# Kernel optimization log

Measured on AMD Instinct MI355X. Metric: run time of the kernel, lower is better.

Reference implementation:

```python
import jax, jax.numpy as jnp
import numpy as np

GROUP = 64      # quantization group size along the K (in_features) dim
QMAX = 7.0      # symmetric signed int4 range [-7, 7]


def fake_quant_w4a4(t):
    """Per-group symmetric int4 fake-quantization along last dim (STE-friendly).

    t: [..., K] with K % GROUP == 0. Emulates nunchaku's quantize_w4a4
    numerics: scale = max|group| / 7, q = clip(round(t/scale)) * scale.
    """
    shp = t.shape
    g = t.reshape(shp[:-1] + (shp[-1] // GROUP, GROUP))
    scale = jnp.maximum(jnp.max(jnp.abs(g), axis=-1, keepdims=True) / QMAX, 1e-8)
    q = jnp.clip(jnp.round(g / scale), -QMAX, QMAX) * scale
    # straight-through estimator so gradients flow through the quant branch
    q = g + jax.lax.stop_gradient(q - g)
    return q.reshape(shp)


def setup_inputs() -> dict:
    key = jax.random.key(0)
    k0, k1, k2, k3, k4, k5 = jax.random.split(key, 6)
    B, K, N, R = 8192, 2048, 2048, 32  # tokens, in_features, out_features, rank
    x = jax.random.normal(k0, (B, K), jnp.float32)
    residual_weight = jax.random.normal(k1, (N, K), jnp.float32) * 0.02
    lora_down = jax.random.normal(k2, (K, R), jnp.float32) * 0.02
    lora_up = jax.random.normal(k3, (N, R), jnp.float32) * 0.02
    smooth = jax.random.uniform(k4, (K,), jnp.float32, minval=0.5, maxval=2.0)
    bias = jax.random.normal(k5, (N,), jnp.float32) * 0.01
    return {"x": x, "residual_weight": residual_weight, "lora_down": lora_down,
            "lora_up": lora_up, "smooth": smooth, "bias": bias}


def reference(x, residual_weight, lora_down, lora_up, smooth, bias):
    """SVDQuant forward: W4A4 GEMM on the residual weight fused with an
    FP low-rank (SVD) correction and per-channel smoothing.

    y = Q4(x*smooth) @ Q4(W_res).T + (x*smooth) @ lora_down @ lora_up.T + bias
    """
    x_s = x * smooth                                   # [B, K] smoothed activations
    y_lr = (x_s @ lora_down) @ lora_up.T               # [B, R] -> [B, N] low-rank branch
    y_q = fake_quant_w4a4(x_s) @ fake_quant_w4a4(residual_weight).T  # int4xint4 branch
    return y_q + y_lr + bias
```

## Files before the change

kernel.cpp:

```cpp
#include <hip/hip_runtime.h>
#include <stdint.h>


typedef __attribute__((ext_vector_type(8))) short short8;
typedef __attribute__((ext_vector_type(8))) unsigned short ushort8;
typedef __attribute__((ext_vector_type(4))) unsigned short ushort4v;
typedef __attribute__((ext_vector_type(4))) float floatx4;

#define M_TOK 8192
#define K_IN  2048
#define N_OUT 2048
#define RANK  32
#define KC    2112
#define NTILE 33
#define XS_STRIDE 2056
#define XROWS 8

__device__ __forceinline__ unsigned short f2bf(float f) {
  unsigned int u = __float_as_uint(f);
  u += 0x7fff + ((u >> 16) & 1);
  return (unsigned short)(u >> 16);
}

__device__ __forceinline__ void quant8(const float* v, unsigned short* q) {
  float amax = 0.f;
#pragma unroll
  for (int i = 0; i < 8; ++i) amax = fmaxf(amax, fabsf(v[i]));
  amax = fmaxf(amax, __shfl_xor(amax, 1, 64));
  amax = fmaxf(amax, __shfl_xor(amax, 2, 64));
  amax = fmaxf(amax, __shfl_xor(amax, 4, 64));
  float scale = fmaxf(amax / 7.0f, 1e-8f);
#pragma unroll
  for (int i = 0; i < 8; ++i) {
    float qq = rintf(v[i] / scale);
    qq = fminf(fmaxf(qq, -7.f), 7.f);
    q[i] = f2bf(qq * scale);
  }
}

__global__ __launch_bounds__(256) void prep_kernel(const float* __restrict__ x,
                                                   const float* __restrict__ smooth,
                                                   const float* __restrict__ wgt,
                                                   const float* __restrict__ ld,
                                                   const float* __restrict__ lup,
                                                   unsigned short* __restrict__ Xcat,
                                                   unsigned short* __restrict__ Wcat) {
  __shared__ unsigned short xs[XROWS * XS_STRIDE];
  __shared__ float red[4][XROWS][32];
  int tid = threadIdx.x;

  if (blockIdx.x >= 1024) {
    int row = blockIdx.x - 1024;
    const float4* wr = (const float4*)(wgt + (size_t)row * K_IN);
    float4 a0 = wr[tid * 2], a1 = wr[tid * 2 + 1];
    float v[8] = {a0.x, a0.y, a0.z, a0.w, a1.x, a1.y, a1.z, a1.w};
    ushort8 q;
    quant8(v, (unsigned short*)&q);
    *(ushort8*)(Wcat + (size_t)row * KC + tid * 8) = q;
    if (tid < 32)      Wcat[(size_t)row * KC + 2048 + tid] = f2bf(lup[row * RANK + tid]);
    else if (tid < 64) Wcat[(size_t)row * KC + 2048 + tid] = 0;
    return;
  }

  int rowbase = blockIdx.x * XROWS;
  int w = tid >> 6, lane = tid & 63, quad = lane >> 4, l16 = lane & 15;

  const float4* sr = (const float4*)smooth;
  float4 s0 = sr[tid * 2], s1 = sr[tid * 2 + 1];
#pragma unroll 2
  for (int r = 0; r < XROWS; ++r) {
    const float4* xr = (const float4*)(x + (size_t)(rowbase + r) * K_IN);
    float4 a0 = xr[tid * 2], a1 = xr[tid * 2 + 1];
    float v[8] = {a0.x * s0.x, a0.y * s0.y, a0.z * s0.z, a0.w * s0.w,
                  a1.x * s1.x, a1.y * s1.y, a1.z * s1.z, a1.w * s1.w};
    ushort8 q;
    quant8(v, (unsigned short*)&q);
    *(ushort8*)(Xcat + (size_t)(rowbase + r) * KC + tid * 8) = q;
    ushort8 sb;
#pragma unroll
    for (int t = 0; t < 8; ++t) sb[t] = f2bf(v[t]);
    *(ushort8*)(xs + r * XS_STRIDE + tid * 8) = sb;
  }
  if (tid < 128)
    *(unsigned int*)(Xcat + (size_t)(rowbase + (tid >> 4)) * KC + 2080 + (tid & 15) * 2) = 0u;
  __syncthreads();

  floatx4 acc[2];
  acc[0] = (floatx4)0.f;
  acc[1] = (floatx4)0.f;
  int kbase = w * 512;
  int arow = (l16 & 7) * XS_STRIDE;
#pragma unroll 2
  for (int it = 0; it < 16; ++it) {
    int k = kbase + it * 32 + quad * 8;
    short8 af = *(const short8*)(xs + arow + k);
    short8 b0, b1;
#pragma unroll
    for (int j = 0; j < 8; ++j) {
      b0[j] = (short)f2bf(ld[(size_t)(k + j) * RANK + l16]);
      b1[j] = (short)f2bf(ld[(size_t)(k + j) * RANK + 16 + l16]);
    }
    acc[0] = __builtin_amdgcn_mfma_f32_16x16x32_bf16(af, b0, acc[0], 0, 0, 0);
    acc[1] = __builtin_amdgcn_mfma_f32_16x16x32_bf16(af, b1, acc[1], 0, 0, 0);
  }
#pragma unroll
  for (int nt = 0; nt < 2; ++nt)
#pragma unroll
    for (int r = 0; r < 4; ++r) {
      int row = quad * 4 + r;
      if (row < XROWS) red[w][row][nt * 16 + l16] = acc[nt][r];
    }
  __syncthreads();
  if (tid < 64) {
    int rl = tid >> 3, seg = tid & 7;
    ushort4v o;
#pragma unroll
    for (int j = 0; j < 4; ++j) {
      int c = seg * 4 + j;
      float s = red[0][rl][c] + red[1][rl][c] + red[2][rl][c] + red[3][rl][c];
      o[j] = f2bf(s);
    }
    *(ushort4v*)(Xcat + (size_t)(rowbase + rl) * KC + 2048 + seg * 4) = o;
  }
}

__device__ __forceinline__ void gld_lds16(const unsigned short* g, unsigned short* l) {
  __builtin_amdgcn_global_load_lds(
      (const __attribute__((address_space(1))) unsigned int*)g,
      (__attribute__((address_space(3))) unsigned int*)l, 16, 0, 0);
}

__global__ __launch_bounds__(512) void gemm_kernel(const unsigned short* __restrict__ Xcat,
                                                   const unsigned short* __restrict__ Wcat,
                                                   const float* __restrict__ bias,
                                                   float* __restrict__ out) {
  __shared__ unsigned short smem[65536];
  int tid = threadIdx.x;
  int w = tid >> 6, lane = tid & 63, quad = lane >> 4, l16 = lane & 15;
  int wm = w >> 2, wn = w & 3;

  int bid = blockIdx.x;
  int wg = (bid & 7) * 32 + (bid >> 3);
  int bM = (wg >> 3) * 256;
  int bN = (wg & 7) * 256;

  int srow = tid >> 3;
  int csrc = (tid & 7) ^ (srow & 7);
  const unsigned short* Ag = Xcat + (size_t)(bM + srow) * KC + csrc * 8;
  const unsigned short* Bg = Wcat + (size_t)(bN + srow) * KC + csrc * 8;
  int ldsrow = w * 512;

#define STAGE(tt, OFF)                                                        \
  do {                                                                        \
    int k0_ = (tt) * 64;                                                      \
    gld_lds16(Ag + k0_,            smem + (OFF) + ldsrow);                    \
    gld_lds16(Ag + 64 * KC + k0_,  smem + (OFF) + 4096 + ldsrow);             \
    gld_lds16(Ag + 128 * KC + k0_, smem + (OFF) + 8192 + ldsrow);             \
    gld_lds16(Ag + 192 * KC + k0_, smem + (OFF) + 12288 + ldsrow);            \
    gld_lds16(Bg + k0_,            smem + (OFF) + 16384 + ldsrow);            \
    gld_lds16(Bg + 64 * KC + k0_,  smem + (OFF) + 20480 + ldsrow);            \
    gld_lds16(Bg + 128 * KC + k0_, smem + (OFF) + 24576 + ldsrow);            \
    gld_lds16(Bg + 192 * KC + k0_, smem + (OFF) + 28672 + ldsrow);            \
  } while (0)

  int l7 = l16 & 7;
  int ck0 = (quad ^ l7) * 8;
  int ck1 = ((4 + quad) ^ l7) * 8;
  int aoff[8], boff[4];
#pragma unroll
  for (int mt = 0; mt < 8; ++mt) aoff[mt] = (wm * 128 + mt * 16 + l16) * 64;
#pragma unroll
  for (int nt = 0; nt < 4; ++nt) boff[nt] = 16384 + (wn * 64 + nt * 16 + l16) * 64;

  floatx4 acc[8][4];
#pragma unroll
  for (int mt = 0; mt < 8; ++mt)
#pragma unroll
    for (int nt = 0; nt < 4; ++nt) acc[mt][nt] = (floatx4)0.f;

  STAGE(0, 0);
  asm volatile("s_waitcnt vmcnt(0)" ::: "memory");
  __builtin_amdgcn_s_barrier();

#pragma unroll 1
  for (int t = 0; t < NTILE; ++t) {
    unsigned short* sb = smem + (t & 1) * 32768;

    if (t + 1 < NTILE) STAGE(t + 1, ((t + 1) & 1) * 32768);

    short8 b0[4], b1[4], a00[4], a01[4], a10[4], a11[4];

#pragma unroll
    for (int nt = 0; nt < 4; ++nt) b0[nt] = *(const short8*)(sb + boff[nt] + ck0);
#pragma unroll
    for (int mt = 0; mt < 4; ++mt) a00[mt] = *(const short8*)(sb + aoff[mt] + ck0);
#pragma unroll
    for (int mt = 0; mt < 4; ++mt) a01[mt] = *(const short8*)(sb + aoff[mt + 4] + ck0);

    __builtin_amdgcn_s_setprio(1);
#pragma unroll
    for (int mt = 0; mt < 4; ++mt)
#pragma unroll
      for (int nt = 0; nt < 4; ++nt)
        acc[mt][nt] = __builtin_amdgcn_mfma_f32_16x16x32_bf16(a00[mt], b0[nt], acc[mt][nt], 0, 0, 0);
    __builtin_amdgcn_s_setprio(0);

#pragma unroll
    for (int nt = 0; nt < 4; ++nt) b1[nt] = *(const short8*)(sb + boff[nt] + ck1);
#pragma unroll
    for (int mt = 0; mt < 4; ++mt) a10[mt] = *(const short8*)(sb + aoff[mt] + ck1);

    __builtin_amdgcn_s_setprio(1);
#pragma unroll
    for (int mt = 0; mt < 4; ++mt)
#pragma unroll
      for (int nt = 0; nt < 4; ++nt)
        acc[mt + 4][nt] = __builtin_amdgcn_mfma_f32_16x16x32_bf16(a01[mt], b0[nt], acc[mt + 4][nt], 0, 0, 0);
    __builtin_amdgcn_s_setprio(0);

#pragma unroll
    for (int mt = 0; mt < 4; ++mt) a11[mt] = *(const short8*)(sb + aoff[mt + 4] + ck1);

    __builtin_amdgcn_s_setprio(1);
#pragma unroll
    for (int mt = 0; mt < 4; ++mt)
#pragma unroll
      for (int nt = 0; nt < 4; ++nt)
        acc[mt][nt] = __builtin_amdgcn_mfma_f32_16x16x32_bf16(a10[mt], b1[nt], acc[mt][nt], 0, 0, 0);
    __builtin_amdgcn_s_setprio(0);

    __builtin_amdgcn_s_setprio(1);
#pragma unroll
    for (int mt = 0; mt < 4; ++mt)
#pragma unroll
      for (int nt = 0; nt < 4; ++nt)
        acc[mt + 4][nt] = __builtin_amdgcn_mfma_f32_16x16x32_bf16(a11[mt], b1[nt], acc[mt + 4][nt], 0, 0, 0);
    __builtin_amdgcn_s_setprio(0);

    if (t + 1 < NTILE) {
      asm volatile("s_waitcnt vmcnt(0)" ::: "memory");
      __builtin_amdgcn_s_barrier();
      __builtin_amdgcn_sched_barrier(0);
    }
  }
#undef STAGE

#pragma unroll
  for (int nt = 0; nt < 4; ++nt) {
    int col = bN + wn * 64 + nt * 16 + l16;
    float bv = bias[col];
#pragma unroll
    for (int mt = 0; mt < 8; ++mt) {
      int row = bM + wm * 128 + mt * 16 + quad * 4;
#pragma unroll
      for (int r2 = 0; r2 < 4; ++r2)
        out[(size_t)(row + r2) * N_OUT + col] = acc[mt][nt][r2] + bv;
    }
  }
}

extern "C" void kernel_launch(void* const* d_in, const int* in_sizes, int n_in,
                              void* d_out, int out_size, void* d_ws, size_t ws_size,
                              hipStream_t stream) {
  const float* x      = (const float*)d_in[0];
  const float* wgt    = (const float*)d_in[1];
  const float* ld     = (const float*)d_in[2];
  const float* lup    = (const float*)d_in[3];
  const float* smooth = (const float*)d_in[4];
  const float* bias   = (const float*)d_in[5];
  float* out = (float*)d_out;

  unsigned short* Xcat = (unsigned short*)d_ws;
  unsigned short* Wcat = Xcat + (size_t)M_TOK * KC;

  hipLaunchKernelGGL(prep_kernel, dim3(1024 + N_OUT), dim3(256), 0, stream,
                     x, smooth, wgt, ld, lup, Xcat, Wcat);
  hipLaunchKernelGGL(gemm_kernel, dim3((M_TOK / 256) * (N_OUT / 256)), dim3(512), 0, stream,
                     Xcat, Wcat, bias, out);
}
```

Baseline: 203.5 us.

## Shrink GEMM tile to 256x128, K-step 32, triple-buffer LDS for occupancy

```diff
diff --git a/kernel.cpp b/kernel.cpp
--- a/kernel.cpp
+++ b/kernel.cpp
@@ -12,7 +12,7 @@
 #define N_OUT 2048
 #define RANK  32
 #define KC    2112
-#define NTILE 33
+#define NTILE 66
 #define XS_STRIDE 2056
 #define XROWS 8
 
@@ -130,118 +130,83 @@
       (__attribute__((address_space(3))) unsigned int*)l, 16, 0, 0);
 }
 
-__global__ __launch_bounds__(512) void gemm_kernel(const unsigned short* __restrict__ Xcat,
-                                                   const unsigned short* __restrict__ Wcat,
-                                                   const float* __restrict__ bias,
-                                                   float* __restrict__ out) {
-  __shared__ unsigned short smem[65536];
+__global__ __launch_bounds__(512, 4) void gemm_kernel(const unsigned short* __restrict__ Xcat,
+                                                      const unsigned short* __restrict__ Wcat,
+                                                      const float* __restrict__ bias,
+                                                      float* __restrict__ out) {
+  __shared__ unsigned short smem[36864];
   int tid = threadIdx.x;
   int w = tid >> 6, lane = tid & 63, quad = lane >> 4, l16 = lane & 15;
-  int wm = w >> 2, wn = w & 3;
+  int wm = w >> 1, wn = w & 1;
 
   int bid = blockIdx.x;
-  int wg = (bid & 7) * 32 + (bid >> 3);
-  int bM = (wg >> 3) * 256;
-  int bN = (wg & 7) * 256;
-
-  int srow = tid >> 3;
-  int csrc = (tid & 7) ^ (srow & 7);
+  int wg = (bid & 7) * 64 + (bid >> 3);
+  int bM = (wg >> 4) * 256;
+  int bN = (wg & 15) * 128;
+
+  int srow = tid >> 2;
+  int csrc = (tid & 3) ^ ((tid >> 3) & 3);
   const unsigned short* Ag = Xcat + (size_t)(bM + srow) * KC + csrc * 8;
   const unsigned short* Bg = Wcat + (size_t)(bN + srow) * KC + csrc * 8;
-  int ldsrow = w * 512;
+  int ldsw = w * 512;
+
+  int ck = (quad ^ ((l16 >> 1) & 3)) * 8;
+  int aoff[4], boff[4];
+#pragma unroll
+  for (int mt = 0; mt < 4; ++mt) aoff[mt] = (wm * 64 + mt * 16 + l16) * 32 + ck;
+#pragma unroll
+  for (int nt = 0; nt < 4; ++nt) boff[nt] = 8192 + (wn * 64 + nt * 16 + l16) * 32 + ck;
+
+  floatx4 acc[4][4];
+#pragma unroll
+  for (int mt = 0; mt < 4; ++mt)
+#pragma unroll
+    for (int nt = 0; nt < 4; ++nt) acc[mt][nt] = (floatx4)0.f;
+
+  int b0 = 0, b1 = 12288, b2 = 24576;
 
 #define STAGE(tt, OFF)                                                        \
   do {                                                                        \
-    int k0_ = (tt) * 64;                                                      \
-    gld_lds16(Ag + k0_,            smem + (OFF) + ldsrow);                    \
-    gld_lds16(Ag + 64 * KC + k0_,  smem + (OFF) + 4096 + ldsrow);             \
-    gld_lds16(Ag + 128 * KC + k0_, smem + (OFF) + 8192 + ldsrow);             \
-    gld_lds16(Ag + 192 * KC + k0_, smem + (OFF) + 12288 + ldsrow);            \
-    gld_lds16(Bg + k0_,            smem + (OFF) + 16384 + ldsrow);            \
-    gld_lds16(Bg + 64 * KC + k0_,  smem + (OFF) + 20480 + ldsrow);            \
-    gld_lds16(Bg + 128 * KC + k0_, smem + (OFF) + 24576 + ldsrow);            \
-    gld_lds16(Bg + 192 * KC + k0_, smem + (OFF) + 28672 + ldsrow);            \
+    int k0_ = (tt) * 32;                                                      \
+    gld_lds16(Ag + k0_,            smem + (OFF) + ldsw);                      \
+    gld_lds16(Ag + 128 * KC + k0_, smem + (OFF) + 4096 + ldsw);               \
+    gld_lds16(Bg + k0_,            smem + (OFF) + 8192 + ldsw);               \
   } while (0)
 
-  int l7 = l16 & 7;
-  int ck0 = (quad ^ l7) * 8;
-  int ck1 = ((4 + quad) ^ l7) * 8;
-  int aoff[8], boff[4];
-#pragma unroll
-  for (int mt = 0; mt < 8; ++mt) aoff[mt] = (wm * 128 + mt * 16 + l16) * 64;
-#pragma unroll
-  for (int nt = 0; nt < 4; ++nt) boff[nt] = 16384 + (wn * 64 + nt * 16 + l16) * 64;
-
-  floatx4 acc[8][4];
-#pragma unroll
-  for (int mt = 0; mt < 8; ++mt)
-#pragma unroll
-    for (int nt = 0; nt < 4; ++nt) acc[mt][nt] = (floatx4)0.f;
-
   STAGE(0, 0);
-  asm volatile("s_waitcnt vmcnt(0)" ::: "memory");
+  STAGE(1, 12288);
+  asm volatile("s_waitcnt vmcnt(3)" ::: "memory");
   __builtin_amdgcn_s_barrier();
 
 #pragma unroll 1
   for (int t = 0; t < NTILE; ++t) {
-    unsigned short* sb = smem + (t & 1) * 32768;
-
-    if (t + 1 < NTILE) STAGE(t + 1, ((t + 1) & 1) * 32768);
-
-    short8 b0[4], b1[4], a00[4], a01[4], a10[4], a11[4];
-
-#pragma unroll
-    for (int nt = 0; nt < 4; ++nt) b0[nt] = *(const short8*)(sb + boff[nt] + ck0);
-#pragma unroll
-    for (int mt = 0; mt < 4; ++mt) a00[mt] = *(const short8*)(sb + aoff[mt] + ck0);
-#pragma unroll
-    for (int mt = 0; mt < 4; ++mt) a01[mt] = *(const short8*)(sb + aoff[mt + 4] + ck0);
+    unsigned short* sb = smem + b0;
+
+    if (t + 2 < NTILE) STAGE(t + 2, b2);
+
+    short8 a[4], b[4];
+#pragma unroll
+    for (int mt = 0; mt < 4; ++mt) a[mt] = *(const short8*)(sb + aoff[mt]);
+#pragma unroll
+    for (int nt = 0; nt < 4; ++nt) b[nt] = *(const short8*)(sb + boff[nt]);
 
     __builtin_amdgcn_s_setprio(1);
 #pragma unroll
     for (int mt = 0; mt < 4; ++mt)
 #pragma unroll
       for (int nt = 0; nt < 4; ++nt)
-        acc[mt][nt] = __builtin_amdgcn_mfma_f32_16x16x32_bf16(a00[mt], b0[nt], acc[mt][nt], 0, 0, 0);
+        acc[mt][nt] = __builtin_amdgcn_mfma_f32_16x16x32_bf16(a[mt], b[nt], acc[mt][nt], 0, 0, 0);
     __builtin_amdgcn_s_setprio(0);
 
-#pragma unroll
-    for (int nt = 0; nt < 4; ++nt) b1[nt] = *(const short8*)(sb + boff[nt] + ck1);
-#pragma unroll
-    for (int mt = 0; mt < 4; ++mt) a10[mt] = *(const short8*)(sb + aoff[mt] + ck1);
-
-    __builtin_amdgcn_s_setprio(1);
-#pragma unroll
-    for (int mt = 0; mt < 4; ++mt)
-#pragma unroll
-      for (int nt = 0; nt < 4; ++nt)
-        acc[mt + 4][nt] = __builtin_amdgcn_mfma_f32_16x16x32_bf16(a01[mt], b0[nt], acc[mt + 4][nt], 0, 0, 0);
-    __builtin_amdgcn_s_setprio(0);
-
-#pragma unroll
-    for (int mt = 0; mt < 4; ++mt) a11[mt] = *(const short8*)(sb + aoff[mt + 4] + ck1);
-
-    __builtin_amdgcn_s_setprio(1);
-#pragma unroll
-    for (int mt = 0; mt < 4; ++mt)
-#pragma unroll
-      for (int nt = 0; nt < 4; ++nt)
-        acc[mt][nt] = __builtin_amdgcn_mfma_f32_16x16x32_bf16(a10[mt], b1[nt], acc[mt][nt], 0, 0, 0);
-    __builtin_amdgcn_s_setprio(0);
-
-    __builtin_amdgcn_s_setprio(1);
-#pragma unroll
-    for (int mt = 0; mt < 4; ++mt)
-#pragma unroll
-      for (int nt = 0; nt < 4; ++nt)
-        acc[mt + 4][nt] = __builtin_amdgcn_mfma_f32_16x16x32_bf16(a11[mt], b1[nt], acc[mt + 4][nt], 0, 0, 0);
-    __builtin_amdgcn_s_setprio(0);
-
+    if (t < NTILE - 2)
+      asm volatile("s_waitcnt vmcnt(3)" ::: "memory");
+    else if (t == NTILE - 2)
+      asm volatile("s_waitcnt vmcnt(0)" ::: "memory");
     if (t + 1 < NTILE) {
-      asm volatile("s_waitcnt vmcnt(0)" ::: "memory");
       __builtin_amdgcn_s_barrier();
       __builtin_amdgcn_sched_barrier(0);
     }
+    int tmp = b0; b0 = b1; b1 = b2; b2 = tmp;
   }
 #undef STAGE
 
@@ -250,8 +215,8 @@
     int col = bN + wn * 64 + nt * 16 + l16;
     float bv = bias[col];
 #pragma unroll
-    for (int mt = 0; mt < 8; ++mt) {
-      int row = bM + wm * 128 + mt * 16 + quad * 4;
+    for (int mt = 0; mt < 4; ++mt) {
+      int row = bM + wm * 64 + mt * 16 + quad * 4;
 #pragma unroll
       for (int r2 = 0; r2 < 4; ++r2)
         out[(size_t)(row + r2) * N_OUT + col] = acc[mt][nt][r2] + bv;
@@ -275,6 +240,6 @@
 
   hipLaunchKernelGGL(prep_kernel, dim3(1024 + N_OUT), dim3(256), 0, stream,
                      x, smooth, wgt, ld, lup, Xcat, Wcat);
-  hipLaunchKernelGGL(gemm_kernel, dim3((M_TOK / 256) * (N_OUT / 256)), dim3(512), 0, stream,
+  hipLaunchKernelGGL(gemm_kernel, dim3((M_TOK / 256) * (N_OUT / 128)), dim3(512), 0, stream,
                      Xcat, Wcat, bias, out);
 }
```

Measured after the change: 214.6 us. 5.5% more time.
